# Kernel tuning notes

Measured on AMD Instinct MI355X. Metric: run time of the kernel, lower is better.

Reference implementation:

```python
import jax, jax.numpy as jnp
import numpy as np

EPS = 1e-5
C = 128
B = 16384
SYMBIOTIC = 4.0
NUM_PARENTS = 16
CHILDREN_PER_PARENT = 7


def _inverse(v):
    # torch: sort -> rank -> reversed rank -> gather sorted values
    idx0 = np.argsort(v, kind='stable')
    value = v[idx0]
    idx1 = np.argsort(idx0, kind='stable')  # ranks
    idx2 = v.shape[0] - 1 - idx1
    return value[idx2]


def _build_stats():
    counts = np.floor(50000.0 * 0.97 ** np.arange(C)) + 1.0  # long-tailed
    N = counts.sum()
    weight = (N / counts).astype(np.float32)
    prior = np.eye(C, dtype=np.float32)
    for p in range(NUM_PARENTS):
        ch = NUM_PARENTS + CHILDREN_PER_PARENT * p + np.arange(CHILDREN_PER_PARENT)
        prior[p, ch] = 1.0
    prior_me = (prior == 0).astype(np.float32)          # 1 - prior, keep only exact 1s
    prior_ms = prior - np.eye(C, dtype=np.float32)      # prior (0/1) minus eye
    v1_sig = np.log(N / counts - 1.0 + EPS).astype(np.float32)
    v2_sig = _inverse(v1_sig).astype(np.float32)
    v1_sm = np.log(counts / N + EPS).astype(np.float32)
    v2_sm = _inverse(v1_sm).astype(np.float32)
    return weight, prior_me, prior_ms, v1_sig, v2_sig, v1_sm, v2_sm


def setup_inputs() -> dict:
    key = jax.random.key(0)
    k1, k2 = jax.random.split(key)
    weight, prior_me, prior_ms, v1s, v2s, v1m, v2m = _build_stats()
    logits = 0.5 * jax.random.normal(k1, (12, B, C), dtype=jnp.float32)
    target = (jax.random.uniform(k2, (B, C)) < 0.1).astype(jnp.float32)
    return {
        'logits': logits, 'target': target,
        'weight': jnp.asarray(weight),
        'prior_me': jnp.asarray(prior_me), 'prior_ms': jnp.asarray(prior_ms),
        'v1_sigmoid': jnp.asarray(v1s), 'v2_sigmoid': jnp.asarray(v2s),
        'v1_softmax': jnp.asarray(v1m), 'v2_softmax': jnp.asarray(v2m),
    }


def reference(logits, target, weight, prior_me, prior_ms,
              v1_sigmoid, v2_sigmoid, v1_softmax, v2_softmax):
    zero = jnp.zeros_like(v1_sigmoid)
    # experts 0-5: sigmoid variants (long-tailed / balanced / inversed, twice)
    sig_shift = jnp.stack([zero, v1_sigmoid, v1_sigmoid - v2_sigmoid] * 2)  # [6,C]
    a_sig = jax.nn.sigmoid(logits[:6] - sig_shift[:, None, :])
    # experts 6-11: local-softmax variants
    sm_shift = jnp.stack([zero, v1_softmax, v1_softmax - v2_softmax] * 2)   # [6,C]
    e = jnp.exp(logits[6:] + sm_shift[:, None, :])                          # [6,B,C]
    denom = jnp.einsum('ebc,cd->ebd', e, prior_me) + e
    a_sm = e / (denom + EPS)
    acti = jnp.clip(jnp.concatenate([a_sig, a_sm], axis=0), EPS, 1.0 - EPS)  # [12,B,C]
    # weighted BCE per expert, summed
    bce = -weight * (target * jnp.log(acti) + (1.0 - target) * jnp.log(1.0 - acti))
    loss = jnp.sum(jnp.mean(bce, axis=(1, 2)))
    # symbiotic regularizer on experts 3,4,5,9,10,11
    row_sum = jnp.sum(prior_ms, axis=1)                 # [C]
    n_nz = jnp.sum(row_sum > 0).astype(acti.dtype)
    bsz = acti.shape[1]

    def symb(a):  # a: [B,C] activated logits
        def step(acc, xs):
            mask_row, parent = xs                       # [C], [B]
            term = jnp.log1p(jnp.exp(a - parent[:, None]))  # [B,C]
            rs = jnp.sum(mask_row)
            contrib = jnp.where(rs > 0, jnp.sum(term * mask_row) / (bsz * rs), 0.0)
            return acc + contrib, None
        total, _ = jax.lax.scan(step, jnp.float32(0.0), (prior_ms, a.T))
        return total / n_nz

    reg = jax.vmap(symb)(acti[jnp.array([3, 4, 5, 9, 10, 11])])
    return loss + SYMBIOTIC * jnp.sum(reg)
```

## Files before the change

### kernel.cpp

```cpp
#include <hip/hip_runtime.h>
#include <math.h>

#define CC 128
#define BB 16384
#define MEPS 1e-5f
#define NBLK 1024
#define EXPSTR ((size_t)BB * (size_t)CC)
#define LOG2E 1.44269504f
#define LN2   0.69314718f


__device__ __forceinline__ float softplus1(float d) {
    const float u = d * d;
    float p = fmaf(u, 3.4722222e-4f, -5.2083333e-3f);
    p = fmaf(u, p, 0.125f);
    return fmaf(u, p, fmaf(d, 0.5f, 0.69314718f));
}

template <int CTRL>
__device__ __forceinline__ float dpp_addstep(float v) {
    const int o = __builtin_amdgcn_update_dpp(0, __float_as_int(v), CTRL, 0xF, 0xF, true);
    return v + __int_as_float(o);
}

__device__ __forceinline__ float rowsum32(float v) {
    v += __int_as_float(__builtin_amdgcn_ds_swizzle(__float_as_int(v), 0x401F));
    v = dpp_addstep<0x140>(v);
    v = dpp_addstep<0x141>(v);
    v = dpp_addstep<0x4E>(v);
    v = dpp_addstep<0xB1>(v);
    return v;
}

__global__ __launch_bounds__(256, 4) void mel_main(
    const float* __restrict__ logits, const float* __restrict__ target,
    const float* __restrict__ weight,
    const float* __restrict__ v1s, const float* __restrict__ v2s,
    const float* __restrict__ v1m, const float* __restrict__ v2m,
    float* __restrict__ partial)
{
    const int lane = threadIdx.x & 63;
    const int wib  = threadIdx.x >> 6;
    const int wave = blockIdx.x * 4 + wib;
    const int r    = lane >> 5;
    const int c    = lane & 31;
    const size_t ro0 = (size_t)(wave * 2 + r) * CC;
    const size_t ro1 = ro0 + (size_t)8192 * CC;

    const float4 wt4 = ((const float4*)weight)[c];
    const float4 s1v = ((const float4*)v1s)[c];
    const float4 s2v = ((const float4*)v2s)[c];
    const float4 m1v = ((const float4*)v1m)[c];
    const float4 m2v = ((const float4*)v2m)[c];
    const float4 tA  = ((const float4*)(target + ro0))[c];
    const float4 tB  = ((const float4*)(target + ro1))[c];

    const float wl[4]  = {wt4.x * LN2, wt4.y * LN2, wt4.z * LN2, wt4.w * LN2};
    const float s1[4]  = {s1v.x, s1v.y, s1v.z, s1v.w};
    const float sd[4]  = {s1v.x - s2v.x, s1v.y - s2v.y, s1v.z - s2v.z, s1v.w - s2v.w};
    const float m1l[4] = {m1v.x * LOG2E, m1v.y * LOG2E, m1v.z * LOG2E, m1v.w * LOG2E};
    const float mdl[4] = {(m1v.x - m2v.x) * LOG2E, (m1v.y - m2v.y) * LOG2E,
                          (m1v.z - m2v.z) * LOG2E, (m1v.w - m2v.w) * LOG2E};
    const float t0Bv[4] = {tB.x > 0.5f ? 0.f : 1.f, tB.y > 0.5f ? 0.f : 1.f,
                           tB.z > 0.5f ? 0.f : 1.f, tB.w > 0.5f ? 0.f : 1.f};
    const float wzBv[4] = {wt4.x * t0Bv[0], wt4.y * t0Bv[1],
                           wt4.z * t0Bv[2], wt4.w * t0Bv[3]};
    float t0[4] = {tA.x > 0.5f ? 0.f : 1.f, tA.y > 0.5f ? 0.f : 1.f,
                   tA.z > 0.5f ? 0.f : 1.f, tA.w > 0.5f ? 0.f : 1.f};
    float wz[4] = {wt4.x * t0[0], wt4.y * t0[1], wt4.z * t0[2], wt4.w * t0[3]};

    const float childf = (c >= 4) ? 1.f : 0.f;
    int pofs[4];
    #pragma unroll
    for (int k = 0; k < 4; ++k) {
        const int ch = 4 * c + k;
        pofs[k] = (ch >= 16) ? (ch - 16) / 7 : 0;
    }

    __shared__ float lds[4][2][16];
    float* Lp = &lds[wib][r][0];

    const float* pA = logits + ro0;
    const float* pB = logits + ro1;
    float4 cur = ((const float4*)pA)[c];
    float4 b1  = ((const float4*)(pA + EXPSTR))[c];
    const float* ppf = pA + 2 * EXPSTR;

    float accP = 0.f;
    float accS = 0.f;
    int e = 0, si = 0;

    #pragma unroll 1
    for (int i = 0; i < 24; ++i) {
        float4 nxt = b1;
        if (i < 22) nxt = ((const float4*)ppf)[c];
        ppf = (i == 9) ? pB : (ppf + EXPSTR);

        const float x[4] = {cur.x, cur.y, cur.z, cur.w};
        if (e < 6) {
            float q[4], z[4];
            #pragma unroll
            for (int k = 0; k < 4; ++k) {
                const float sh = (si == 0) ? 0.f : ((si == 1) ? s1[k] : sd[k]);
                z[k] = x[k] - sh;
                const float ex = __builtin_amdgcn_exp2f(z[k] * -LOG2E);
                q[k] = 1.f + ex;
                accP = fmaf(wl[k], __builtin_amdgcn_logf(q[k]), accP);
                accP = fmaf(wz[k], z[k], accP);
            }
            if (e >= 3) {
                float a[4];
                #pragma unroll
                for (int k = 0; k < 4; ++k) a[k] = __builtin_amdgcn_rcpf(q[k]);
                if (c < 4) *(float4*)(Lp + 4 * c) = make_float4(a[0], a[1], a[2], a[3]);
                #pragma unroll
                for (int k = 0; k < 4; ++k)
                    accS = fmaf(childf, softplus1(a[k] - Lp[pofs[k]]), accS);
            }
        } else {
            float ek[4];
            float S = 0.f;
            #pragma unroll
            for (int k = 0; k < 4; ++k) {
                const float shl = (si == 0) ? 0.f : ((si == 1) ? m1l[k] : mdl[k]);
                ek[k] = __builtin_amdgcn_exp2f(fmaf(x[k], LOG2E, shl));
                S += ek[k];
            }
            if (c < 4) *(float4*)(Lp + 4 * c) = make_float4(ek[0], ek[1], ek[2], ek[3]);
            const float Sj = rowsum32(S) + MEPS;
            const float rS = __builtin_amdgcn_rcpf(Sj);
            #pragma unroll
            for (int k = 0; k < 4; ++k) {
                const float ep  = Lp[pofs[k]];
                const float den = fmaf(childf, -ep, Sj);
                float a = ek[k] * __builtin_amdgcn_rcpf(den);
                a = fminf(fmaxf(a, MEPS), 1.f - MEPS);
                const float arg = fmaf(t0[k], fmaf(-2.f, a, 1.f), a);
                accP = fmaf(wl[k], -__builtin_amdgcn_logf(arg), accP);
                if (e >= 9)
                    accS = fmaf(childf, softplus1(fmaf(ep, -rS, a)), accS);
            }
        }

        cur = b1; b1 = nxt;
        ++e; ++si;
        if (si == 3) si = 0;
        if (e == 12) {
            e = 0;
            #pragma unroll
            for (int k = 0; k < 4; ++k) { t0[k] = t0Bv[k]; wz[k] = wzBv[k]; }
        }
    }

    float val = accP * (1.f / ((float)BB * (float)CC))
              + accS * (4.f / (112.f * (float)BB));

    #pragma unroll
    for (int off = 32; off > 0; off >>= 1)
        val += __shfl_xor(val, off, 64);

    __shared__ float sdata[4];
    if (lane == 0) sdata[wib] = val;
    __syncthreads();
    if (threadIdx.x == 0)
        partial[blockIdx.x] = (sdata[0] + sdata[1]) + (sdata[2] + sdata[3]);
}

__global__ __launch_bounds__(256) void mel_reduce(
    const float* __restrict__ partial, float* __restrict__ out)
{
    float v = 0.f;
    #pragma unroll
    for (int i = 0; i < NBLK / 256; ++i)
        v += partial[threadIdx.x + i * 256];
    #pragma unroll
    for (int off = 32; off > 0; off >>= 1)
        v += __shfl_xor(v, off, 64);
    __shared__ float s[4];
    const int lane = threadIdx.x & 63, wib = threadIdx.x >> 6;
    if (lane == 0) s[wib] = v;
    __syncthreads();
    if (threadIdx.x == 0) out[0] = (s[0] + s[1]) + (s[2] + s[3]);
}

extern "C" void kernel_launch(void* const* d_in, const int* in_sizes, int n_in,
                              void* d_out, int out_size, void* d_ws, size_t ws_size,
                              hipStream_t stream) {
    const float* logits = (const float*)d_in[0];
    const float* target = (const float*)d_in[1];
    const float* weight = (const float*)d_in[2];
    const float* v1s = (const float*)d_in[5];
    const float* v2s = (const float*)d_in[6];
    const float* v1m = (const float*)d_in[7];
    const float* v2m = (const float*)d_in[8];
    float* partial = (float*)d_ws;
    float* out = (float*)d_out;

    mel_main<<<NBLK, 256, 0, stream>>>(logits, target, weight,
                                       v1s, v2s, v1m, v2m, partial);
    mel_reduce<<<1, 256, 0, stream>>>(partial, out);
}
```

Before: 166.6 us.

## Assign each wave a fixed expert pair over 16 rows instead of all experts

Work is redistributed so each wave handles one sigmoid expert and its matching softmax expert (duo) across 16 rows, rather than all 12 experts for two rows. Shift vectors and the symbiotic flag become wave-uniform constants, which removes per-iteration select logic, and the grid grows to 1536 blocks with a 6-block occupancy hint. The cost is that target rows are now reloaded per iteration (and re-read by each of six duos) instead of being loaded once, and register pressure under the tighter launch bound may force spills.

Measured after the change: 169.9 us. No clear change (+2.0%).

```diff
diff --git a/kernel.cpp b/kernel.cpp
--- a/kernel.cpp
+++ b/kernel.cpp
@@ -4,7 +4,7 @@
 #define CC 128
 #define BB 16384
 #define MEPS 1e-5f
-#define NBLK 1024
+#define NBLK 1536
 #define EXPSTR ((size_t)BB * (size_t)CC)
 #define LOG2E 1.44269504f
 #define LN2   0.69314718f
@@ -32,7 +32,7 @@
     return v;
 }
 
-__global__ __launch_bounds__(256, 4) void mel_main(
+__global__ __launch_bounds__(256, 6) void mel_main(
     const float* __restrict__ logits, const float* __restrict__ target,
     const float* __restrict__ weight,
     const float* __restrict__ v1s, const float* __restrict__ v2s,
@@ -42,32 +42,33 @@
     const int lane = threadIdx.x & 63;
     const int wib  = threadIdx.x >> 6;
     const int wave = blockIdx.x * 4 + wib;
+    const int duo  = wave >> 10;
+    const int g    = wave & 1023;
     const int r    = lane >> 5;
     const int c    = lane & 31;
-    const size_t ro0 = (size_t)(wave * 2 + r) * CC;
-    const size_t ro1 = ro0 + (size_t)8192 * CC;
+    const bool symb = (duo >= 3);
+    const int si   = symb ? duo - 3 : duo;
 
     const float4 wt4 = ((const float4*)weight)[c];
     const float4 s1v = ((const float4*)v1s)[c];
     const float4 s2v = ((const float4*)v2s)[c];
     const float4 m1v = ((const float4*)v1m)[c];
     const float4 m2v = ((const float4*)v2m)[c];
-    const float4 tA  = ((const float4*)(target + ro0))[c];
-    const float4 tB  = ((const float4*)(target + ro1))[c];
-
-    const float wl[4]  = {wt4.x * LN2, wt4.y * LN2, wt4.z * LN2, wt4.w * LN2};
-    const float s1[4]  = {s1v.x, s1v.y, s1v.z, s1v.w};
-    const float sd[4]  = {s1v.x - s2v.x, s1v.y - s2v.y, s1v.z - s2v.z, s1v.w - s2v.w};
-    const float m1l[4] = {m1v.x * LOG2E, m1v.y * LOG2E, m1v.z * LOG2E, m1v.w * LOG2E};
-    const float mdl[4] = {(m1v.x - m2v.x) * LOG2E, (m1v.y - m2v.y) * LOG2E,
-                          (m1v.z - m2v.z) * LOG2E, (m1v.w - m2v.w) * LOG2E};
-    const float t0Bv[4] = {tB.x > 0.5f ? 0.f : 1.f, tB.y > 0.5f ? 0.f : 1.f,
-                           tB.z > 0.5f ? 0.f : 1.f, tB.w > 0.5f ? 0.f : 1.f};
-    const float wzBv[4] = {wt4.x * t0Bv[0], wt4.y * t0Bv[1],
-                           wt4.z * t0Bv[2], wt4.w * t0Bv[3]};
-    float t0[4] = {tA.x > 0.5f ? 0.f : 1.f, tA.y > 0.5f ? 0.f : 1.f,
-                   tA.z > 0.5f ? 0.f : 1.f, tA.w > 0.5f ? 0.f : 1.f};
-    float wz[4] = {wt4.x * t0[0], wt4.y * t0[1], wt4.z * t0[2], wt4.w * t0[3]};
+
+    float wl[4], sh[4], shl[4];
+    {
+        const float a1[4] = {s1v.x, s1v.y, s1v.z, s1v.w};
+        const float a2[4] = {s1v.x - s2v.x, s1v.y - s2v.y, s1v.z - s2v.z, s1v.w - s2v.w};
+        const float b1v[4] = {m1v.x, m1v.y, m1v.z, m1v.w};
+        const float b2v[4] = {m1v.x - m2v.x, m1v.y - m2v.y, m1v.z - m2v.z, m1v.w - m2v.w};
+        const float wtv[4] = {wt4.x, wt4.y, wt4.z, wt4.w};
+        #pragma unroll
+        for (int k = 0; k < 4; ++k) {
+            wl[k]  = wtv[k] * LN2;
+            sh[k]  = (si == 0) ? 0.f : ((si == 1) ? a1[k] : a2[k]);
+            shl[k] = ((si == 0) ? 0.f : ((si == 1) ? b1v[k] : b2v[k])) * LOG2E;
+        }
+    }
 
     const float childf = (c >= 4) ? 1.f : 0.f;
     int pofs[4];
@@ -80,35 +81,46 @@
     __shared__ float lds[4][2][16];
     float* Lp = &lds[wib][r][0];
 
-    const float* pA = logits + ro0;
-    const float* pB = logits + ro1;
-    float4 cur = ((const float4*)pA)[c];
-    float4 b1  = ((const float4*)(pA + EXPSTR))[c];
-    const float* ppf = pA + 2 * EXPSTR;
+    const size_t rowoff = ((size_t)(16 * g) + (size_t)r) * CC;
+    const float* LA = logits + (size_t)duo * EXPSTR + rowoff;
+    const float* LB = LA + (size_t)6 * EXPSTR;
+    const float* Tb = target + rowoff;
+
+    float4 cur = ((const float4*)LA)[c];
+    float4 b1  = ((const float4*)(LA + 2 * CC))[c];
+    float4 tc  = ((const float4*)Tb)[c];
+    float4 tb  = ((const float4*)(Tb + 2 * CC))[c];
 
     float accP = 0.f;
     float accS = 0.f;
-    int e = 0, si = 0;
 
     #pragma unroll 1
-    for (int i = 0; i < 24; ++i) {
-        float4 nxt = b1;
-        if (i < 22) nxt = ((const float4*)ppf)[c];
-        ppf = (i == 9) ? pB : (ppf + EXPSTR);
-
-        const float x[4] = {cur.x, cur.y, cur.z, cur.w};
-        if (e < 6) {
-            float q[4], z[4];
+    for (int i = 0; i < 16; ++i) {
+        float4 nL = b1, nT = tb;
+        if (i < 14) {
+            const int j = i + 2;
+            const int off = (j & 7) * (2 * CC);
+            const float* lb = (j & 8) ? LB : LA;
+            nL = ((const float4*)(lb + off))[c];
+            nT = ((const float4*)(Tb + off))[c];
+        }
+
+        const float x[4]  = {cur.x, cur.y, cur.z, cur.w};
+        const float t0[4] = {tc.x > 0.5f ? 0.f : 1.f, tc.y > 0.5f ? 0.f : 1.f,
+                             tc.z > 0.5f ? 0.f : 1.f, tc.w > 0.5f ? 0.f : 1.f};
+
+        if (i < 8) {
+            float q[4];
             #pragma unroll
             for (int k = 0; k < 4; ++k) {
-                const float sh = (si == 0) ? 0.f : ((si == 1) ? s1[k] : sd[k]);
-                z[k] = x[k] - sh;
-                const float ex = __builtin_amdgcn_exp2f(z[k] * -LOG2E);
+                const float z = x[k] - sh[k];
+                const float m = z * -LOG2E;
+                const float ex = __builtin_amdgcn_exp2f(m);
                 q[k] = 1.f + ex;
                 accP = fmaf(wl[k], __builtin_amdgcn_logf(q[k]), accP);
-                accP = fmaf(wz[k], z[k], accP);
-            }
-            if (e >= 3) {
+                accP = fmaf(wl[k] * t0[k], -m, accP);
+            }
+            if (symb) {
                 float a[4];
                 #pragma unroll
                 for (int k = 0; k < 4; ++k) a[k] = __builtin_amdgcn_rcpf(q[k]);
@@ -122,13 +134,13 @@
             float S = 0.f;
             #pragma unroll
             for (int k = 0; k < 4; ++k) {
-                const float shl = (si == 0) ? 0.f : ((si == 1) ? m1l[k] : mdl[k]);
-                ek[k] = __builtin_amdgcn_exp2f(fmaf(x[k], LOG2E, shl));
+                ek[k] = __builtin_amdgcn_exp2f(fmaf(x[k], LOG2E, shl[k]));
                 S += ek[k];
             }
             if (c < 4) *(float4*)(Lp + 4 * c) = make_float4(ek[0], ek[1], ek[2], ek[3]);
             const float Sj = rowsum32(S) + MEPS;
-            const float rS = __builtin_amdgcn_rcpf(Sj);
+            float rS = 0.f;
+            if (symb) rS = __builtin_amdgcn_rcpf(Sj);
             #pragma unroll
             for (int k = 0; k < 4; ++k) {
                 const float ep  = Lp[pofs[k]];
@@ -137,19 +149,13 @@
                 a = fminf(fmaxf(a, MEPS), 1.f - MEPS);
                 const float arg = fmaf(t0[k], fmaf(-2.f, a, 1.f), a);
                 accP = fmaf(wl[k], -__builtin_amdgcn_logf(arg), accP);
-                if (e >= 9)
+                if (symb)
                     accS = fmaf(childf, softplus1(fmaf(ep, -rS, a)), accS);
             }
         }
 
-        cur = b1; b1 = nxt;
-        ++e; ++si;
-        if (si == 3) si = 0;
-        if (e == 12) {
-            e = 0;
-            #pragma unroll
-            for (int k = 0; k < 4; ++k) { t0[k] = t0Bv[k]; wz[k] = wzBv[k]; }
-        }
+        cur = b1; b1 = nL;
+        tc  = tb; tb = nT;
     }
 
     float val = accP * (1.f / ((float)BB * (float)CC))
```
